# Kernel optimization log

Measured on AMD Instinct MI355X. Metric: run time of the kernel, lower is better.

Reference implementation:

```python
import jax, jax.numpy as jnp
import numpy as np

N = 50000        # nodes
E = 800000       # edges
IN_C = 128       # in_channels
HID = 256        # hidden_channels
HEADS = 4
HD = HID // HEADS
LAYERS = 4
GRAPHS = 64
OUT_C = 32
MAX_POS = 10
EPS = 1e-5


def layer_norm(x, g, b):
    mu = jnp.mean(x, axis=-1, keepdims=True)
    var = jnp.mean((x - mu) ** 2, axis=-1, keepdims=True)
    return (x - mu) / jnp.sqrt(var + EPS) * g + b


def setup_inputs() -> dict:
    key = jax.random.key(0)
    ks = jax.random.split(key, 32)
    s = 0.02
    inp = {
        "x": jax.random.normal(ks[0], (N, IN_C), dtype=jnp.float32),
        "edge_index": jax.random.randint(ks[1], (2, E), 0, N, dtype=jnp.int32),
        "pos_idx": jax.random.randint(ks[2], (N,), 0, MAX_POS, dtype=jnp.int32),
        "batch": jnp.sort(jax.random.randint(ks[3], (N,), 0, GRAPHS, dtype=jnp.int32)),
        # encoder MLP: Linear(IN->HID), ReLU, LN(HID), Linear(HID->HID); weights stored [in,out]
        "enc_w1": jax.random.normal(ks[4], (IN_C, HID)) * s,
        "enc_b1": jnp.zeros((HID,), jnp.float32),
        "enc_g": jnp.ones((HID,), jnp.float32),
        "enc_beta": jnp.zeros((HID,), jnp.float32),
        "enc_w2": jax.random.normal(ks[5], (HID, HID)) * s,
        "enc_b2": jnp.zeros((HID,), jnp.float32),
        "pos_emb": jax.random.normal(ks[6], (MAX_POS, HID)) * s,
        # stacked attention-layer params [LAYERS, ...]
        "Wq": jax.random.normal(ks[7], (LAYERS, HID, HID)) * s,
        "bq": jnp.zeros((LAYERS, HID), jnp.float32),
        "Wk": jax.random.normal(ks[8], (LAYERS, HID, HID)) * s,
        "bk": jnp.zeros((LAYERS, HID), jnp.float32),
        "Wv": jax.random.normal(ks[9], (LAYERS, HID, HID)) * s,
        "bv": jnp.zeros((LAYERS, HID), jnp.float32),
        "mlp_w1": jax.random.normal(ks[10], (LAYERS, 2 * HID, HID)) * s,
        "mlp_b1": jnp.zeros((LAYERS, HID), jnp.float32),
        "mlp_g": jnp.ones((LAYERS, HID), jnp.float32),
        "mlp_beta": jnp.zeros((LAYERS, HID), jnp.float32),
        "mlp_w2": jax.random.normal(ks[11], (LAYERS, HID, HID)) * s,
        "mlp_b2": jnp.zeros((LAYERS, HID), jnp.float32),
        # classifier
        "cls_w1": jax.random.normal(ks[12], (HID, HID)) * s,
        "cls_b1": jnp.zeros((HID,), jnp.float32),
        "cls_g": jnp.ones((HID,), jnp.float32),
        "cls_beta": jnp.zeros((HID,), jnp.float32),
        "cls_w2": jax.random.normal(ks[13], (HID, OUT_C)) * s,
        "cls_b2": jnp.zeros((OUT_C,), jnp.float32),
    }
    return inp


def reference(x, edge_index, pos_idx, batch,
              enc_w1, enc_b1, enc_g, enc_beta, enc_w2, enc_b2, pos_emb,
              Wq, bq, Wk, bk, Wv, bv,
              mlp_w1, mlp_b1, mlp_g, mlp_beta, mlp_w2, mlp_b2,
              cls_w1, cls_b1, cls_g, cls_beta, cls_w2, cls_b2):
    row, col = edge_index[0], edge_index[1]
    n = x.shape[0]
    e = row.shape[0]

    # NodeEncoder
    h = layer_norm(jax.nn.relu(x @ enc_w1 + enc_b1), enc_g, enc_beta) @ enc_w2 + enc_b2
    h = h + pos_emb[pos_idx]

    scale = jnp.asarray(HD, h.dtype) ** 0.5
    for l in range(LAYERS):
        Q = (h @ Wq[l] + bq[l]).reshape(n, HEADS, HD)
        K = (h @ Wk[l] + bk[l]).reshape(n, HEADS, HD)
        V = (h @ Wv[l] + bv[l]).reshape(n, HEADS, HD)
        # per-edge attention scores [E, HEADS]
        scores = jnp.sum(Q[row] * K[col], axis=-1) / scale
        # segment softmax over destination node `row`
        m = jax.ops.segment_max(scores, row, num_segments=n)
        ex = jnp.exp(scores - m[row])
        denom = jax.ops.segment_sum(ex, row, num_segments=n)
        w = ex / denom[row]                         # [E, HEADS]
        msg = (w[..., None] * V[col]).reshape(e, HID)
        agg = jax.ops.segment_sum(msg, row, num_segments=n)  # [N, HID]
        cat = jnp.concatenate([h, agg], axis=-1)
        z = layer_norm(jax.nn.relu(cat @ mlp_w1[l] + mlp_b1[l]), mlp_g[l], mlp_beta[l]) @ mlp_w2[l] + mlp_b2[l]
        h = z + h

    # global mean pool over graphs
    sums = jax.ops.segment_sum(h, batch, num_segments=GRAPHS)
    cnt = jax.ops.segment_sum(jnp.ones((n, 1), h.dtype), batch, num_segments=GRAPHS)
    pooled = sums / jnp.maximum(cnt, 1.0)

    out = layer_norm(jax.nn.relu(pooled @ cls_w1 + cls_b1), cls_g, cls_beta) @ cls_w2 + cls_b2
    return out
```

## Files before the change

### kernel.cpp

```cpp
#include <hip/hip_runtime.h>
#include <cstdint>

#define HID 256
#define HEADS 4
#define GRAPHS 64
#define OUTC 32
#define EPSV 1e-5f
#define PSPLIT 32

typedef __bf16 b16x8 __attribute__((ext_vector_type(8)));
typedef float  f32x4 __attribute__((ext_vector_type(4)));

__device__ __forceinline__ f32x4 mfma16(b16x8 a, b16x8 b, f32x4 c) {
    return __builtin_amdgcn_mfma_f32_16x16x32_bf16(a, b, c, 0, 0, 0);
}

__device__ __forceinline__ unsigned int pack_bf16(float a, float b) {
    unsigned short ua = __builtin_bit_cast(unsigned short, (__bf16)a);
    unsigned short ub = __builtin_bit_cast(unsigned short, (__bf16)b);
    return (unsigned int)ua | ((unsigned int)ub << 16);
}

__device__ __forceinline__ void unpack2(unsigned int u, float& lo, float& hi) {
    lo = __builtin_bit_cast(float, u << 16);
    hi = __builtin_bit_cast(float, u & 0xffff0000u);
}

__global__ __launch_bounds__(256) void wtrans_kernel(const float* __restrict__ W,
    unsigned short* __restrict__ Wt, int K, int C)
{
    __shared__ float tile[32][33];
    const float* Wm = W + (size_t)blockIdx.z * K * C;
    unsigned short* Wtm = Wt + (size_t)blockIdx.z * K * C;
    int k0 = blockIdx.x * 32, c0 = blockIdx.y * 32;
    int tx = threadIdx.x & 31, ty = threadIdx.x >> 5;
#pragma unroll
    for (int i = 0; i < 32; i += 8)
        tile[ty + i][tx] = Wm[(size_t)(k0 + ty + i) * C + c0 + tx];
    __syncthreads();
#pragma unroll
    for (int i = 0; i < 32; i += 8) {
        float v = tile[tx][ty + i];
        Wtm[(size_t)(c0 + ty + i) * K + k0 + tx] =
            __builtin_bit_cast(unsigned short, (__bf16)v);
    }
}

__global__ __launch_bounds__(256) void enc1_mfma(
    const float* __restrict__ in0, const unsigned short* __restrict__ Wt,
    const float* __restrict__ bias, const float* __restrict__ g,
    const float* __restrict__ be, unsigned short* __restrict__ outb, int n)
{
    constexpr int KTILE = 128, ROWB = 256;
    __shared__ __align__(16) char alds[64 * 256];
    __shared__ float red[4][64][2];
    int tid = threadIdx.x, lane = tid & 63, wv = tid >> 6;
    int cg = lane & 15, rg = lane >> 4;
    int base = blockIdx.x * 64;
    int cbase = wv * 64;

    f32x4 acc[4][4];
#pragma unroll
    for (int m = 0; m < 4; m++)
#pragma unroll
        for (int f = 0; f < 4; f++) acc[m][f] = (f32x4){0.f, 0.f, 0.f, 0.f};

#pragma unroll
    for (int i = 0; i < 8; i++) {
        int idx = (i * 256 + tid) * 4;
        int row = idx >> 7, k = idx & 127;
        int node = base + row;
        float4 v = {0.f, 0.f, 0.f, 0.f};
        if (node < n) v = *(const float4*)(in0 + (size_t)node * KTILE + k);
        uint2 pp; pp.x = pack_bf16(v.x, v.y); pp.y = pack_bf16(v.z, v.w);
        int off = row * ROWB + k * 2;
        off ^= (row & 7) << 4;
        *(uint2*)(alds + off) = pp;
    }
    __syncthreads();

#pragma unroll 2
    for (int k0 = 0; k0 < KTILE; k0 += 32) {
        b16x8 a[4], b[4];
#pragma unroll
        for (int m = 0; m < 4; m++) {
            int R = m * 16 + cg;
            int off = R * ROWB + (k0 + rg * 8) * 2;
            off ^= (R & 7) << 4;
            a[m] = __builtin_bit_cast(b16x8, *(const uint4*)(alds + off));
        }
#pragma unroll
        for (int f = 0; f < 4; f++) {
            const unsigned short* p = Wt + (size_t)(cbase + f * 16 + cg) * KTILE + k0 + rg * 8;
            b[f] = __builtin_bit_cast(b16x8, *(const uint4*)p);
        }
#pragma unroll
        for (int m = 0; m < 4; m++)
#pragma unroll
            for (int f = 0; f < 4; f++)
                acc[m][f] = mfma16(a[m], b[f], acc[m][f]);
    }

    float bias_v[4], g_v[4], be_v[4];
#pragma unroll
    for (int f = 0; f < 4; f++) {
        int col = cbase + f * 16 + cg;
        bias_v[f] = bias[col]; g_v[f] = g[col]; be_v[f] = be[col];
    }
#pragma unroll
    for (int m = 0; m < 4; m++)
#pragma unroll
        for (int f = 0; f < 4; f++)
#pragma unroll
            for (int r = 0; r < 4; r++)
                acc[m][f][r] = fmaxf(acc[m][f][r] + bias_v[f], 0.f);
#pragma unroll
    for (int m = 0; m < 4; m++)
#pragma unroll
        for (int r = 0; r < 4; r++) {
            float s = acc[m][0][r] + acc[m][1][r] + acc[m][2][r] + acc[m][3][r];
            float q = acc[m][0][r] * acc[m][0][r] + acc[m][1][r] * acc[m][1][r]
                    + acc[m][2][r] * acc[m][2][r] + acc[m][3][r] * acc[m][3][r];
#pragma unroll
            for (int o = 1; o < 16; o <<= 1) {
                s += __shfl_xor(s, o, 64); q += __shfl_xor(q, o, 64);
            }
            if (cg == 0) { int R = m * 16 + rg * 4 + r; red[wv][R][0] = s; red[wv][R][1] = q; }
        }
    __syncthreads();
#pragma unroll
    for (int m = 0; m < 4; m++)
#pragma unroll
        for (int r = 0; r < 4; r++) {
            int R = m * 16 + rg * 4 + r;
            float S = red[0][R][0] + red[1][R][0] + red[2][R][0] + red[3][R][0];
            float Q = red[0][R][1] + red[1][R][1] + red[2][R][1] + red[3][R][1];
            float mu = S * (1.f / HID);
            float rs = rsqrtf(Q * (1.f / HID) - mu * mu + EPSV);
            int row = base + R;
            if (row >= n) continue;
            size_t ro = (size_t)row * HID;
#pragma unroll
            for (int f = 0; f < 4; f++) {
                float v = (acc[m][f][r] - mu) * rs * g_v[f] + be_v[f];
                outb[ro + cbase + f * 16 + cg] = __builtin_bit_cast(unsigned short, (__bf16)v);
            }
        }
}

template<int KTILE, int NPASS, bool RELU_LN, bool ADD_RES, bool POS, bool OUTF, bool OUTB>
__global__ __launch_bounds__(256) void gemm_bf16(
    const unsigned short* __restrict__ in0, const unsigned short* __restrict__ in1,
    const unsigned short* __restrict__ Wt, const float* __restrict__ bias,
    const float* __restrict__ g, const float* __restrict__ be,
    const float* __restrict__ addsrc, const float* __restrict__ pos_emb,
    const int* __restrict__ pidx, float* __restrict__ outf,
    unsigned short* __restrict__ outb, int n)
{
    constexpr int KS = KTILE * NPASS;
    constexpr int ROWB = KTILE * 2;
    constexpr int UPR = KTILE / 8;
    __shared__ __align__(16) char alds[64 * KTILE * 2];
    __shared__ float red[4][64][2];

    int tid = threadIdx.x, lane = tid & 63, wv = tid >> 6;
    int cg = lane & 15, rg = lane >> 4;
    int base = blockIdx.x * 64;
    int cbase = wv * 64;

    f32x4 acc[4][4];
#pragma unroll
    for (int m = 0; m < 4; m++)
#pragma unroll
        for (int f = 0; f < 4; f++) acc[m][f] = (f32x4){0.f, 0.f, 0.f, 0.f};

    for (int pass = 0; pass < NPASS; pass++) {
        if (pass) __syncthreads();
        const unsigned short* src = pass ? in1 : in0;
        constexpr int ITERS = (64 * UPR) / 256;
#pragma unroll
        for (int i = 0; i < ITERS; i++) {
            int idx = i * 256 + tid;
            int row = idx / UPR, u = idx % UPR;
            int node = base + row;
            uint4 v = {0u, 0u, 0u, 0u};
            if (node < n) v = *(const uint4*)(src + (size_t)node * KTILE + u * 8);
            int off = row * ROWB + u * 16;
            off ^= (row & 7) << 4;
            *(uint4*)(alds + off) = v;
        }
        __syncthreads();

        const unsigned short* Wp = Wt + pass * KTILE;
#pragma unroll 2
        for (int k0 = 0; k0 < KTILE; k0 += 32) {
            b16x8 a[4], b[4];
#pragma unroll
            for (int m = 0; m < 4; m++) {
                int R = m * 16 + cg;
                int off = R * ROWB + (k0 + rg * 8) * 2;
                off ^= (R & 7) << 4;
                a[m] = __builtin_bit_cast(b16x8, *(const uint4*)(alds + off));
            }
#pragma unroll
            for (int f = 0; f < 4; f++) {
                const unsigned short* p = Wp + (size_t)(cbase + f * 16 + cg) * KS + k0 + rg * 8;
                b[f] = __builtin_bit_cast(b16x8, *(const uint4*)p);
            }
#pragma unroll
            for (int m = 0; m < 4; m++)
#pragma unroll
                for (int f = 0; f < 4; f++)
                    acc[m][f] = mfma16(a[m], b[f], acc[m][f]);
        }
    }

    float bias_v[4], g_v[4], be_v[4];
#pragma unroll
    for (int f = 0; f < 4; f++) {
        int col = cbase + f * 16 + cg;
        bias_v[f] = bias[col];
        if (RELU_LN) { g_v[f] = g[col]; be_v[f] = be[col]; }
    }
#pragma unroll
    for (int m = 0; m < 4; m++)
#pragma unroll
        for (int f = 0; f < 4; f++)
#pragma unroll
            for (int r = 0; r < 4; r++) acc[m][f][r] += bias_v[f];

    if (RELU_LN) {
#pragma unroll
        for (int m = 0; m < 4; m++)
#pragma unroll
            for (int f = 0; f < 4; f++)
#pragma unroll
                for (int r = 0; r < 4; r++) acc[m][f][r] = fmaxf(acc[m][f][r], 0.f);
#pragma unroll
        for (int m = 0; m < 4; m++)
#pragma unroll
            for (int r = 0; r < 4; r++) {
                float s = acc[m][0][r] + acc[m][1][r] + acc[m][2][r] + acc[m][3][r];
                float q = acc[m][0][r] * acc[m][0][r] + acc[m][1][r] * acc[m][1][r]
                        + acc[m][2][r] * acc[m][2][r] + acc[m][3][r] * acc[m][3][r];
#pragma unroll
                for (int o = 1; o < 16; o <<= 1) {
                    s += __shfl_xor(s, o, 64); q += __shfl_xor(q, o, 64);
                }
                if (cg == 0) { int R = m * 16 + rg * 4 + r; red[wv][R][0] = s; red[wv][R][1] = q; }
            }
        __syncthreads();
#pragma unroll
        for (int m = 0; m < 4; m++)
#pragma unroll
            for (int r = 0; r < 4; r++) {
                int R = m * 16 + rg * 4 + r;
                float S = red[0][R][0] + red[1][R][0] + red[2][R][0] + red[3][R][0];
                float Q = red[0][R][1] + red[1][R][1] + red[2][R][1] + red[3][R][1];
                float mu = S * (1.f / HID);
                float rs = rsqrtf(Q * (1.f / HID) - mu * mu + EPSV);
#pragma unroll
                for (int f = 0; f < 4; f++)
                    acc[m][f][r] = (acc[m][f][r] - mu) * rs * g_v[f] + be_v[f];
            }
    }

#pragma unroll
    for (int m = 0; m < 4; m++)
#pragma unroll
        for (int r = 0; r < 4; r++) {
            int row = base + m * 16 + rg * 4 + r;
            if (row >= n) continue;
            size_t ro = (size_t)row * HID;
            int pid = 0;
            if (POS) pid = pidx[row];
#pragma unroll
            for (int f = 0; f < 4; f++) {
                int col = cbase + f * 16 + cg;
                float v = acc[m][f][r];
                if (ADD_RES) v += addsrc[ro + col];
                if (POS)     v += pos_emb[(size_t)pid * HID + col];
                if (OUTF)    outf[ro + col] = v;
                if (OUTB)    outb[ro + col] = __builtin_bit_cast(unsigned short, (__bf16)v);
            }
        }
}

__global__ __launch_bounds__(256) void qkv_mfma_kernel(
    const unsigned short* __restrict__ hsrc,
    const unsigned short* __restrict__ Wtq, const unsigned short* __restrict__ Wtk,
    const unsigned short* __restrict__ Wtv,
    const float* __restrict__ bq, const float* __restrict__ bk, const float* __restrict__ bv,
    unsigned short* __restrict__ Qo, unsigned short* __restrict__ Ko,
    unsigned short* __restrict__ Vo, int n)
{
    constexpr int ROWB = 512;
    __shared__ __align__(16) char alds[64 * 512];
    int tid = threadIdx.x, lane = tid & 63, wv = tid >> 6;
    int cg = lane & 15, rg = lane >> 4;
    int base = blockIdx.x * 64;
    int cbase = wv * 64;

#pragma unroll
    for (int i = 0; i < 8; i++) {
        int idx = i * 256 + tid;
        int row = idx >> 5, u = idx & 31;
        int node = base + row;
        uint4 v = {0u, 0u, 0u, 0u};
        if (node < n) v = *(const uint4*)(hsrc + (size_t)node * HID + u * 8);
        int off = row * ROWB + u * 16;
        off ^= (row & 7) << 4;
        *(uint4*)(alds + off) = v;
    }
    __syncthreads();

    for (int mat = 0; mat < 3; mat++) {
        const unsigned short* Wp = (mat == 0) ? Wtq : (mat == 1) ? Wtk : Wtv;
        const float* bp = (mat == 0) ? bq : (mat == 1) ? bk : bv;
        unsigned short* op = (mat == 0) ? Qo : (mat == 1) ? Ko : Vo;

        f32x4 acc[4][4];
#pragma unroll
        for (int m = 0; m < 4; m++)
#pragma unroll
            for (int f = 0; f < 4; f++) acc[m][f] = (f32x4){0.f, 0.f, 0.f, 0.f};

#pragma unroll 2
        for (int k0 = 0; k0 < 256; k0 += 32) {
            b16x8 a[4], b[4];
#pragma unroll
            for (int m = 0; m < 4; m++) {
                int R = m * 16 + cg;
                int off = R * ROWB + (k0 + rg * 8) * 2;
                off ^= (R & 7) << 4;
                a[m] = __builtin_bit_cast(b16x8, *(const uint4*)(alds + off));
            }
#pragma unroll
            for (int f = 0; f < 4; f++) {
                const unsigned short* p = Wp + (size_t)(cbase + f * 16 + cg) * 256 + k0 + rg * 8;
                b[f] = __builtin_bit_cast(b16x8, *(const uint4*)p);
            }
#pragma unroll
            for (int m = 0; m < 4; m++)
#pragma unroll
                for (int f = 0; f < 4; f++)
                    acc[m][f] = mfma16(a[m], b[f], acc[m][f]);
        }

        float bias_v[4];
#pragma unroll
        for (int f = 0; f < 4; f++) bias_v[f] = bp[cbase + f * 16 + cg];
#pragma unroll
        for (int m = 0; m < 4; m++)
#pragma unroll
            for (int r = 0; r < 4; r++) {
                int row = base + m * 16 + rg * 4 + r;
                if (row >= n) continue;
                size_t ro = (size_t)row * HID;
#pragma unroll
                for (int f = 0; f < 4; f++) {
                    float v = acc[m][f][r] + bias_v[f];
                    op[ro + cbase + f * 16 + cg] = __builtin_bit_cast(unsigned short, (__bf16)v);
                }
            }
    }
}

__global__ void count_kernel(const int* __restrict__ row, int* __restrict__ counts, int e)
{
    int i = blockIdx.x * blockDim.x + threadIdx.x;
    if (i < e) atomicAdd(&counts[row[i]], 1);
}

__global__ __launch_bounds__(256) void scan1_kernel(const int* __restrict__ counts,
    int* __restrict__ offs, int* __restrict__ bsum, int n)
{
    __shared__ int wsumS[4];
    int tid = threadIdx.x, b = blockIdx.x;
    int i = b * 256 + tid;
    int v = (i < n) ? counts[i] : 0;
    int lane = tid & 63, wv = tid >> 6;
    int s = v;
#pragma unroll
    for (int o = 1; o < 64; o <<= 1) { int t = __shfl_up(s, o, 64); if (lane >= o) s += t; }
    if (lane == 63) wsumS[wv] = s;
    __syncthreads();
    int add = 0;
    for (int j = 0; j < wv; j++) add += wsumS[j];
    s += add;
    if (i < n) offs[i + 1] = s;
    if (tid == 255) bsum[b] = s;
}

__global__ __launch_bounds__(256) void scan2_kernel(int* __restrict__ bsum, int nb)
{
    __shared__ int wsumS[4];
    int tid = threadIdx.x;
// ... 43 lines not shown
    int hw = (wv << 1) | (lane >> 5);
    int l32 = lane & 31;
    int grp = l32 >> 3;
    int start = offs[node], fin = offs[node + 1];
    if (fin == start) {
        agg[(size_t)node * HID + tid] = 0;
        return;
    }

    uint4 qr = *(const uint4*)(Qm + (size_t)node * HID + l32 * 8);
    float qf[8];
    unpack2(qr.x, qf[0], qf[1]);
    unpack2(qr.y, qf[2], qf[3]);
    unpack2(qr.z, qf[4], qf[5]);
    unpack2(qr.w, qf[6], qf[7]);

    float m = -3.0e38f, d = 0.f;
    float acc[8];
#pragma unroll
    for (int j = 0; j < 8; j++) acc[j] = 0.f;

    for (int i = start + hw; i < fin; i += 8) {
        int c = ccol[i];
        uint4 kr = *(const uint4*)(Km + (size_t)c * HID + l32 * 8);
        float k0, k1, k2, k3, k4, k5, k6, k7;
        unpack2(kr.x, k0, k1); unpack2(kr.y, k2, k3);
        unpack2(kr.z, k4, k5); unpack2(kr.w, k6, k7);
        float p = qf[0] * k0 + qf[1] * k1 + qf[2] * k2 + qf[3] * k3
                + qf[4] * k4 + qf[5] * k5 + qf[6] * k6 + qf[7] * k7;
        p += __shfl_xor(p, 1, 64);
        p += __shfl_xor(p, 2, 64);
        p += __shfl_xor(p, 4, 64);
        float s = p * 0.125f;
        float mn = fmaxf(m, s);
        float sc = __expf(m - mn);
        float w = __expf(s - mn);
        d = d * sc + w;
        uint4 vr = *(const uint4*)(Vm + (size_t)c * HID + l32 * 8);
        float v0, v1, v2, v3, v4, v5, v6, v7;
        unpack2(vr.x, v0, v1); unpack2(vr.y, v2, v3);
        unpack2(vr.z, v4, v5); unpack2(vr.w, v6, v7);
        acc[0] = acc[0] * sc + w * v0;  acc[1] = acc[1] * sc + w * v1;
        acc[2] = acc[2] * sc + w * v2;  acc[3] = acc[3] * sc + w * v3;
        acc[4] = acc[4] * sc + w * v4;  acc[5] = acc[5] * sc + w * v5;
        acc[6] = acc[6] * sc + w * v6;  acc[7] = acc[7] * sc + w * v7;
        m = mn;
    }
    if ((l32 & 7) == 0) { wredM[hw][grp] = m; wredD[hw][grp] = d; }
    __syncthreads();
    float M = wredM[0][grp];
#pragma unroll
    for (int j = 1; j < 8; j++) M = fmaxf(M, wredM[j][grp]);
    float fac = __expf(m - M);
    float4 a0 = {acc[0] * fac, acc[1] * fac, acc[2] * fac, acc[3] * fac};
    float4 a1 = {acc[4] * fac, acc[5] * fac, acc[6] * fac, acc[7] * fac};
    *(float4*)&accT[hw][l32 * 8]     = a0;
    *(float4*)&accT[hw][l32 * 8 + 4] = a1;
    __syncthreads();
    int hh = tid >> 6;
    float M2 = wredM[0][hh];
#pragma unroll
    for (int j = 1; j < 8; j++) M2 = fmaxf(M2, wredM[j][hh]);
    float D = 0.f;
#pragma unroll
    for (int j = 0; j < 8; j++) D += wredD[j][hh] * __expf(wredM[j][hh] - M2);
    float r = 0.f;
#pragma unroll
    for (int j = 0; j < 8; j++) r += accT[j][tid];
    agg[(size_t)node * HID + tid] = __builtin_bit_cast(unsigned short, (__bf16)(r / D));
}

__global__ void bounds_kernel(const int* __restrict__ batch, int* __restrict__ gb, int n)
{
    int g = threadIdx.x;
    if (g > GRAPHS) return;
    int lo = 0, hi = n;
    while (lo < hi) { int mid = (lo + hi) >> 1; if (batch[mid] < g) lo = mid + 1; else hi = mid; }
    gb[g] = lo;
}
// ... 72 lines not shown
    const float* bq       = (const float*)d_in[12];
    const float* Wk       = (const float*)d_in[13];
    const float* bk       = (const float*)d_in[14];
    const float* Wv       = (const float*)d_in[15];
    const float* bv       = (const float*)d_in[16];
    const float* mlp_w1   = (const float*)d_in[17];
    const float* mlp_b1   = (const float*)d_in[18];
    const float* mlp_g    = (const float*)d_in[19];
    const float* mlp_beta = (const float*)d_in[20];
    const float* mlp_w2   = (const float*)d_in[21];
    const float* mlp_b2   = (const float*)d_in[22];
    const float* cls_w1   = (const float*)d_in[23];
    const float* cls_b1   = (const float*)d_in[24];
    const float* cls_g    = (const float*)d_in[25];
    const float* cls_beta = (const float*)d_in[26];
    const float* cls_w2   = (const float*)d_in[27];
    const float* cls_b2   = (const float*)d_in[28];

    int n = in_sizes[2];
    int e = in_sizes[1] / 2;
    const int* row = ei;
    const int* col = ei + e;

    char* p = (char*)d_ws;
    auto alloc = [&](size_t bytes) -> void* {
        void* r = (void*)p;
        p += (bytes + 255) & ~(size_t)255;
        return r;
    };
    size_t NH = (size_t)n * HID;
    float* h             = (float*)alloc(NH * 4);
    unsigned short* h16  = (unsigned short*)alloc(NH * 2);
    unsigned short* a16  = (unsigned short*)alloc(NH * 2);
    unsigned short* m16  = (unsigned short*)alloc(NH * 2);
    unsigned short* Qb   = (unsigned short*)alloc(NH * 2);
    unsigned short* Kb   = (unsigned short*)alloc(NH * 2);
    unsigned short* Vb   = (unsigned short*)alloc(NH * 2);
    float* partial = (float*)alloc((size_t)GRAPHS * PSPLIT * HID * 4);
    float* pooled  = (float*)alloc((size_t)GRAPHS * HID * 4);
    int* counts = (int*)alloc((size_t)n * 4);
    int* offs   = (int*)alloc((size_t)(n + 1) * 4);
    int* cur    = (int*)alloc((size_t)n * 4);
    int* ccol   = (int*)alloc((size_t)e * 4);
    int* bsum   = (int*)alloc(1024);
    int* gb     = (int*)alloc((GRAPHS + 1) * 4);
    unsigned short* wt_e1 = (unsigned short*)alloc((size_t)128 * 256 * 2);
    unsigned short* wt_e2 = (unsigned short*)alloc((size_t)256 * 256 * 2);
    unsigned short* wt_q  = (unsigned short*)alloc((size_t)4 * 256 * 256 * 2);
    unsigned short* wt_k  = (unsigned short*)alloc((size_t)4 * 256 * 256 * 2);
    unsigned short* wt_v  = (unsigned short*)alloc((size_t)4 * 256 * 256 * 2);
    unsigned short* wt_m1 = (unsigned short*)alloc((size_t)4 * 512 * 256 * 2);
    unsigned short* wt_m2 = (unsigned short*)alloc((size_t)4 * 256 * 256 * 2);

    int gblocks = (n + 63) / 64;
    int nb = (n + 255) / 256;

    wtrans_kernel<<<dim3(4, 8, 1),  256, 0, stream>>>(enc_w1, wt_e1, 128, 256);
    wtrans_kernel<<<dim3(8, 8, 1),  256, 0, stream>>>(enc_w2, wt_e2, 256, 256);
    wtrans_kernel<<<dim3(8, 8, 4),  256, 0, stream>>>(Wq,     wt_q,  256, 256);
    wtrans_kernel<<<dim3(8, 8, 4),  256, 0, stream>>>(Wk,     wt_k,  256, 256);
    wtrans_kernel<<<dim3(8, 8, 4),  256, 0, stream>>>(Wv,     wt_v,  256, 256);
    wtrans_kernel<<<dim3(16, 8, 4), 256, 0, stream>>>(mlp_w1, wt_m1, 512, 256);
    wtrans_kernel<<<dim3(8, 8, 4),  256, 0, stream>>>(mlp_w2, wt_m2, 256, 256);

    hipMemsetAsync(counts, 0, (size_t)n * 4, stream);
    hipMemsetAsync(cur, 0, (size_t)n * 4, stream);
    count_kernel<<<(e + 255) / 256, 256, 0, stream>>>(row, counts, e);
    scan1_kernel<<<nb, 256, 0, stream>>>(counts, offs, bsum, n);
    scan2_kernel<<<1, 256, 0, stream>>>(bsum, nb);
    scan3_kernel<<<nb, 256, 0, stream>>>(offs, bsum, n);
    scatter_kernel<<<(e + 255) / 256, 256, 0, stream>>>(row, col, offs, cur, ccol, e);
    bounds_kernel<<<1, 128, 0, stream>>>(batch, gb, n);

    enc1_mfma<<<gblocks, 256, 0, stream>>>(x, wt_e1, enc_b1, enc_g, enc_beta, m16, n);
    gemm_bf16<256, 1, false, false, true, true, true><<<gblocks, 256, 0, stream>>>(
        m16, nullptr, wt_e2, enc_b2, nullptr, nullptr, nullptr, pos_emb, pidx, h, h16, n);

    for (int l = 0; l < 4; l++) {
        size_t wo = (size_t)l * 256 * 256;
        size_t bo = (size_t)l * HID;
        qkv_mfma_kernel<<<gblocks, 256, 0, stream>>>(
            h16, wt_q + wo, wt_k + wo, wt_v + wo, bq + bo, bk + bo, bv + bo,
            Qb, Kb, Vb, n);
        attn_bf16_kernel<<<n, 256, 0, stream>>>(Qb, Kb, Vb, offs, ccol, a16, n);
        gemm_bf16<256, 2, true, false, false, false, true><<<gblocks, 256, 0, stream>>>(
            h16, a16, wt_m1 + (size_t)l * 512 * 256, mlp_b1 + bo,
            mlp_g + bo, mlp_beta + bo, nullptr, nullptr, nullptr, nullptr, m16, n);
        gemm_bf16<256, 1, false, true, false, true, true><<<gblocks, 256, 0, stream>>>(
            m16, nullptr, wt_m2 + wo, mlp_b2 + bo, nullptr, nullptr, h, nullptr, nullptr,
            h, h16, n);
    }

    pool_partial_kernel<<<dim3(PSPLIT, GRAPHS), 256, 0, stream>>>(h, gb, partial);
    pool_reduce_kernel<<<GRAPHS, 256, 0, stream>>>(partial, gb, pooled);
    cls_kernel<<<GRAPHS, 256, 0, stream>>>(pooled, cls_w1, cls_b1, cls_g, cls_beta,
                                           cls_w2, cls_b2, (float*)d_out);
}
```

Baseline: 1.419 ms.

## Fuse encoder, per-layer MLP and next-layer QKV GEMMs into single kernels

The two encoder GEMMs and the first QKV projection become one kernel, and each layer's two MLP GEMMs plus the next layer's QKV projection become another. Intermediate tiles stay in LDS instead of being written to and re-read from global memory, and several launches per layer are dropped. Separately, the online softmax in the attention kernel now rescales its accumulators only when the running max rises by more than 8, which skips most rescale multiplies. The cost is a longer serial kernel per block with larger LDS use, and the lazy rescale lets the exp weights grow up to e^8 before renormalising.

Result: slower. 1.495 ms (+5.3%).

```diff
diff --git a/kernel.cpp b/kernel.cpp
--- a/kernel.cpp
+++ b/kernel.cpp
@@ -26,72 +26,38 @@
     hi = __builtin_bit_cast(float, u & 0xffff0000u);
 }
 
-__global__ __launch_bounds__(256) void wtrans_kernel(const float* __restrict__ W,
-    unsigned short* __restrict__ Wt, int K, int C)
-{
-    __shared__ float tile[32][33];
-    const float* Wm = W + (size_t)blockIdx.z * K * C;
-    unsigned short* Wtm = Wt + (size_t)blockIdx.z * K * C;
-    int k0 = blockIdx.x * 32, c0 = blockIdx.y * 32;
-    int tx = threadIdx.x & 31, ty = threadIdx.x >> 5;
-#pragma unroll
-    for (int i = 0; i < 32; i += 8)
-        tile[ty + i][tx] = Wm[(size_t)(k0 + ty + i) * C + c0 + tx];
-    __syncthreads();
-#pragma unroll
-    for (int i = 0; i < 32; i += 8) {
-        float v = tile[tx][ty + i];
-        Wtm[(size_t)(c0 + ty + i) * K + k0 + tx] =
-            __builtin_bit_cast(unsigned short, (__bf16)v);
-    }
-}
-
-__global__ __launch_bounds__(256) void enc1_mfma(
-    const float* __restrict__ in0, const unsigned short* __restrict__ Wt,
-    const float* __restrict__ bias, const float* __restrict__ g,
-    const float* __restrict__ be, unsigned short* __restrict__ outb, int n)
-{
-    constexpr int KTILE = 128, ROWB = 256;
-    __shared__ __align__(16) char alds[64 * 256];
-    __shared__ float red[4][64][2];
-    int tid = threadIdx.x, lane = tid & 63, wv = tid >> 6;
-    int cg = lane & 15, rg = lane >> 4;
-    int base = blockIdx.x * 64;
-    int cbase = wv * 64;
-
-    f32x4 acc[4][4];
-#pragma unroll
-    for (int m = 0; m < 4; m++)
-#pragma unroll
-        for (int f = 0; f < 4; f++) acc[m][f] = (f32x4){0.f, 0.f, 0.f, 0.f};
-
+__device__ __forceinline__ void stage_b16(char* buf, const unsigned short* src,
+                                          int base, int n, int tid)
+{
 #pragma unroll
     for (int i = 0; i < 8; i++) {
-        int idx = (i * 256 + tid) * 4;
-        int row = idx >> 7, k = idx & 127;
+        int idx = i * 256 + tid;
+        int row = idx >> 5, u = idx & 31;
         int node = base + row;
-        float4 v = {0.f, 0.f, 0.f, 0.f};
-        if (node < n) v = *(const float4*)(in0 + (size_t)node * KTILE + k);
-        uint2 pp; pp.x = pack_bf16(v.x, v.y); pp.y = pack_bf16(v.z, v.w);
-        int off = row * ROWB + k * 2;
+        uint4 v = {0u, 0u, 0u, 0u};
+        if (node < n) v = *(const uint4*)(src + (size_t)node * HID + u * 8);
+        int off = row * 512 + u * 16;
         off ^= (row & 7) << 4;
-        *(uint2*)(alds + off) = pp;
-    }
-    __syncthreads();
-
+        *(uint4*)(buf + off) = v;
+    }
+}
+
+__device__ __forceinline__ void pass256(const char* buf, const unsigned short* Wt,
+    int KS, int cbase, int cg, int rg, f32x4 (&acc)[4][4])
+{
 #pragma unroll 2
-    for (int k0 = 0; k0 < KTILE; k0 += 32) {
+    for (int k0 = 0; k0 < 256; k0 += 32) {
         b16x8 a[4], b[4];
 #pragma unroll
         for (int m = 0; m < 4; m++) {
             int R = m * 16 + cg;
-            int off = R * ROWB + (k0 + rg * 8) * 2;
+            int off = R * 512 + (k0 + rg * 8) * 2;
             off ^= (R & 7) << 4;
-            a[m] = __builtin_bit_cast(b16x8, *(const uint4*)(alds + off));
+            a[m] = __builtin_bit_cast(b16x8, *(const uint4*)(buf + off));
         }
 #pragma unroll
         for (int f = 0; f < 4; f++) {
-            const unsigned short* p = Wt + (size_t)(cbase + f * 16 + cg) * KTILE + k0 + rg * 8;
+            const unsigned short* p = Wt + (size_t)(cbase + f * 16 + cg) * KS + k0 + rg * 8;
             b[f] = __builtin_bit_cast(b16x8, *(const uint4*)p);
         }
 #pragma unroll
@@ -100,12 +66,16 @@
             for (int f = 0; f < 4; f++)
                 acc[m][f] = mfma16(a[m], b[f], acc[m][f]);
     }
-
-    float bias_v[4], g_v[4], be_v[4];
+}
+
+__device__ __forceinline__ void tile_bias_relu_ln(f32x4 (&acc)[4][4], float (*red)[64][2],
+    const float* bias, const float* g, const float* be, int cbase, int cg, int rg, int wv)
+{
+    float b_v[4], g_v[4], be_v[4];
 #pragma unroll
     for (int f = 0; f < 4; f++) {
         int col = cbase + f * 16 + cg;
-        bias_v[f] = bias[col]; g_v[f] = g[col]; be_v[f] = be[col];
+        b_v[f] = bias[col]; g_v[f] = g[col]; be_v[f] = be[col];
     }
 #pragma unroll
     for (int m = 0; m < 4; m++)
@@ -113,7 +83,7 @@
         for (int f = 0; f < 4; f++)
 #pragma unroll
             for (int r = 0; r < 4; r++)
-                acc[m][f][r] = fmaxf(acc[m][f][r] + bias_v[f], 0.f);
+                acc[m][f][r] = fmaxf(acc[m][f][r] + b_v[f], 0.f);
 #pragma unroll
     for (int m = 0; m < 4; m++)
 #pragma unroll
@@ -137,216 +107,154 @@
             float Q = red[0][R][1] + red[1][R][1] + red[2][R][1] + red[3][R][1];
             float mu = S * (1.f / HID);
             float rs = rsqrtf(Q * (1.f / HID) - mu * mu + EPSV);
-            int row = base + R;
-            if (row >= n) continue;
-            size_t ro = (size_t)row * HID;
+#pragma unroll
+            for (int f = 0; f < 4; f++)
+                acc[m][f][r] = (acc[m][f][r] - mu) * rs * g_v[f] + be_v[f];
+        }
+}
+
+__device__ __forceinline__ void put_tile(char* buf, const f32x4 (&acc)[4][4],
+    int cbase, int cg, int rg)
+{
+#pragma unroll
+    for (int m = 0; m < 4; m++)
+#pragma unroll
+        for (int r = 0; r < 4; r++) {
+            int R = m * 16 + rg * 4 + r;
 #pragma unroll
             for (int f = 0; f < 4; f++) {
-                float v = (acc[m][f][r] - mu) * rs * g_v[f] + be_v[f];
-                outb[ro + cbase + f * 16 + cg] = __builtin_bit_cast(unsigned short, (__bf16)v);
+                int col = cbase + f * 16 + cg;
+                int off = R * 512 + col * 2;
+                off ^= (R & 7) << 4;
+                *(unsigned short*)(buf + off) =
+                    __builtin_bit_cast(unsigned short, (__bf16)acc[m][f][r]);
             }
         }
 }
 
-template<int KTILE, int NPASS, bool RELU_LN, bool ADD_RES, bool POS, bool OUTF, bool OUTB>
-__global__ __launch_bounds__(256) void gemm_bf16(
-    const unsigned short* __restrict__ in0, const unsigned short* __restrict__ in1,
-    const unsigned short* __restrict__ Wt, const float* __restrict__ bias,
-    const float* __restrict__ g, const float* __restrict__ be,
-    const float* __restrict__ addsrc, const float* __restrict__ pos_emb,
-    const int* __restrict__ pidx, float* __restrict__ outf,
-    unsigned short* __restrict__ outb, int n)
-{
-    constexpr int KS = KTILE * NPASS;
-    constexpr int ROWB = KTILE * 2;
-    constexpr int UPR = KTILE / 8;
-    __shared__ __align__(16) char alds[64 * KTILE * 2];
+__device__ __forceinline__ void zero_acc(f32x4 (&acc)[4][4])
+{
+#pragma unroll
+    for (int m = 0; m < 4; m++)
+#pragma unroll
+        for (int f = 0; f < 4; f++) acc[m][f] = (f32x4){0.f, 0.f, 0.f, 0.f};
+}
+
+__global__ __launch_bounds__(256) void wtrans_kernel(const float* __restrict__ W,
+    unsigned short* __restrict__ Wt, int K, int C)
+{
+    __shared__ float tile[32][33];
+    const float* Wm = W + (size_t)blockIdx.z * K * C;
+    unsigned short* Wtm = Wt + (size_t)blockIdx.z * K * C;
+    int k0 = blockIdx.x * 32, c0 = blockIdx.y * 32;
+    int tx = threadIdx.x & 31, ty = threadIdx.x >> 5;
+#pragma unroll
+    for (int i = 0; i < 32; i += 8)
+        tile[ty + i][tx] = Wm[(size_t)(k0 + ty + i) * C + c0 + tx];
+    __syncthreads();
+#pragma unroll
+    for (int i = 0; i < 32; i += 8) {
+        float v = tile[tx][ty + i];
+        Wtm[(size_t)(c0 + ty + i) * K + k0 + tx] =
+            __builtin_bit_cast(unsigned short, (__bf16)v);
+    }
+}
+
+__global__ __launch_bounds__(256) void enc_fused(
+    const float* __restrict__ x,
+    const unsigned short* __restrict__ wt_e1, const float* __restrict__ eb1,
+    const float* __restrict__ eg, const float* __restrict__ ebe,
+    const unsigned short* __restrict__ wt_e2, const float* __restrict__ eb2,
+    const float* __restrict__ pos_emb, const int* __restrict__ pidx,
+    const unsigned short* __restrict__ wtq, const unsigned short* __restrict__ wtk,
+    const unsigned short* __restrict__ wtv,
+    const float* __restrict__ bqv, const float* __restrict__ bkv, const float* __restrict__ bvv,
+    float* __restrict__ h, unsigned short* __restrict__ h16,
+    unsigned short* __restrict__ Qo, unsigned short* __restrict__ Ko,
+    unsigned short* __restrict__ Vo, int n)
+{
+    __shared__ __align__(16) char buf[64 * 512];
     __shared__ float red[4][64][2];
-
     int tid = threadIdx.x, lane = tid & 63, wv = tid >> 6;
     int cg = lane & 15, rg = lane >> 4;
     int base = blockIdx.x * 64;
     int cbase = wv * 64;
 
+#pragma unroll
+    for (int i = 0; i < 8; i++) {
+        int idx = (i * 256 + tid) * 4;
+        int row = idx >> 7, k = idx & 127;
+        int node = base + row;
+        float4 v = {0.f, 0.f, 0.f, 0.f};
+        if (node < n) v = *(const float4*)(x + (size_t)node * 128 + k);
+        uint2 pp; pp.x = pack_bf16(v.x, v.y); pp.y = pack_bf16(v.z, v.w);
+        int off = row * 256 + k * 2;
+        off ^= (row & 7) << 4;
+        *(uint2*)(buf + off) = pp;
+    }
+    __syncthreads();
+
     f32x4 acc[4][4];
-#pragma unroll
-    for (int m = 0; m < 4; m++)
-#pragma unroll
-        for (int f = 0; f < 4; f++) acc[m][f] = (f32x4){0.f, 0.f, 0.f, 0.f};
-
-    for (int pass = 0; pass < NPASS; pass++) {
-        if (pass) __syncthreads();
-        const unsigned short* src = pass ? in1 : in0;
-        constexpr int ITERS = (64 * UPR) / 256;
-#pragma unroll
-        for (int i = 0; i < ITERS; i++) {
-            int idx = i * 256 + tid;
-            int row = idx / UPR, u = idx % UPR;
-            int node = base + row;
-            uint4 v = {0u, 0u, 0u, 0u};
-            if (node < n) v = *(const uint4*)(src + (size_t)node * KTILE + u * 8);
-            int off = row * ROWB + u * 16;
-            off ^= (row & 7) << 4;
-            *(uint4*)(alds + off) = v;
-        }
-        __syncthreads();
-
-        const unsigned short* Wp = Wt + pass * KTILE;
+    zero_acc(acc);
 #pragma unroll 2
-        for (int k0 = 0; k0 < KTILE; k0 += 32) {
-            b16x8 a[4], b[4];
-#pragma unroll
-            for (int m = 0; m < 4; m++) {
-                int R = m * 16 + cg;
-                int off = R * ROWB + (k0 + rg * 8) * 2;
-                off ^= (R & 7) << 4;
-                a[m] = __builtin_bit_cast(b16x8, *(const uint4*)(alds + off));
-            }
-#pragma unroll
-            for (int f = 0; f < 4; f++) {
-                const unsigned short* p = Wp + (size_t)(cbase + f * 16 + cg) * KS + k0 + rg * 8;
-                b[f] = __builtin_bit_cast(b16x8, *(const uint4*)p);
-            }
-#pragma unroll
-            for (int m = 0; m < 4; m++)
-#pragma unroll
-                for (int f = 0; f < 4; f++)
-                    acc[m][f] = mfma16(a[m], b[f], acc[m][f]);
-        }
-    }
-
-    float bias_v[4], g_v[4], be_v[4];
-#pragma unroll
-    for (int f = 0; f < 4; f++) {
-        int col = cbase + f * 16 + cg;
-        bias_v[f] = bias[col];
-        if (RELU_LN) { g_v[f] = g[col]; be_v[f] = be[col]; }
-    }
-#pragma unroll
-    for (int m = 0; m < 4; m++)
-#pragma unroll
-        for (int f = 0; f < 4; f++)
-#pragma unroll
-            for (int r = 0; r < 4; r++) acc[m][f][r] += bias_v[f];
-
-    if (RELU_LN) {
+    for (int k0 = 0; k0 < 128; k0 += 32) {
+        b16x8 a[4], b[4];
+#pragma unroll
+        for (int m = 0; m < 4; m++) {
+            int R = m * 16 + cg;
+            int off = R * 256 + (k0 + rg * 8) * 2;
+            off ^= (R & 7) << 4;
+            a[m] = __builtin_bit_cast(b16x8, *(const uint4*)(buf + off));
+        }
+#pragma unroll
+        for (int f = 0; f < 4; f++) {
+            const unsigned short* p = wt_e1 + (size_t)(cbase + f * 16 + cg) * 128 + k0 + rg * 8;
+            b[f] = __builtin_bit_cast(b16x8, *(const uint4*)p);
+        }
 #pragma unroll
         for (int m = 0; m < 4; m++)
 #pragma unroll
             for (int f = 0; f < 4; f++)
-#pragma unroll
-                for (int r = 0; r < 4; r++) acc[m][f][r] = fmaxf(acc[m][f][r], 0.f);
-#pragma unroll
-        for (int m = 0; m < 4; m++)
-#pragma unroll
-            for (int r = 0; r < 4; r++) {
-                float s = acc[m][0][r] + acc[m][1][r] + acc[m][2][r] + acc[m][3][r];
-                float q = acc[m][0][r] * acc[m][0][r] + acc[m][1][r] * acc[m][1][r]
-                        + acc[m][2][r] * acc[m][2][r] + acc[m][3][r] * acc[m][3][r];
-#pragma unroll
-                for (int o = 1; o < 16; o <<= 1) {
-                    s += __shfl_xor(s, o, 64); q += __shfl_xor(q, o, 64);
-                }
-                if (cg == 0) { int R = m * 16 + rg * 4 + r; red[wv][R][0] = s; red[wv][R][1] = q; }
-            }
-        __syncthreads();
-#pragma unroll
-        for (int m = 0; m < 4; m++)
-#pragma unroll
-            for (int r = 0; r < 4; r++) {
-                int R = m * 16 + rg * 4 + r;
-                float S = red[0][R][0] + red[1][R][0] + red[2][R][0] + red[3][R][0];
-                float Q = red[0][R][1] + red[1][R][1] + red[2][R][1] + red[3][R][1];
-                float mu = S * (1.f / HID);
-                float rs = rsqrtf(Q * (1.f / HID) - mu * mu + EPSV);
-#pragma unroll
-                for (int f = 0; f < 4; f++)
-                    acc[m][f][r] = (acc[m][f][r] - mu) * rs * g_v[f] + be_v[f];
-            }
-    }
-
+                acc[m][f] = mfma16(a[m], b[f], acc[m][f]);
+    }
+    tile_bias_relu_ln(acc, red, eb1, eg, ebe, cbase, cg, rg, wv);
+    put_tile(buf, acc, cbase, cg, rg);
+    __syncthreads();
+
+    zero_acc(acc);
+    pass256(buf, wt_e2, 256, cbase, cg, rg, acc);
+    float b2_v[4];
+#pragma unroll
+    for (int f = 0; f < 4; f++) b2_v[f] = eb2[cbase + f * 16 + cg];
 #pragma unroll
     for (int m = 0; m < 4; m++)
 #pragma unroll
         for (int r = 0; r < 4; r++) {
             int row = base + m * 16 + rg * 4 + r;
-            if (row >= n) continue;
+            bool ok = row < n;
+            int pid = ok ? pidx[row] : 0;
             size_t ro = (size_t)row * HID;
-            int pid = 0;
-            if (POS) pid = pidx[row];
 #pragma unroll
             for (int f = 0; f < 4; f++) {
                 int col = cbase + f * 16 + cg;
-                float v = acc[m][f][r];
-                if (ADD_RES) v += addsrc[ro + col];
-                if (POS)     v += pos_emb[(size_t)pid * HID + col];
-                if (OUTF)    outf[ro + col] = v;
-                if (OUTB)    outb[ro + col] = __builtin_bit_cast(unsigned short, (__bf16)v);
+                float v = acc[m][f][r] + b2_v[f] + pos_emb[(size_t)pid * HID + col];
+                acc[m][f][r] = v;
+                if (ok) {
+                    h[ro + col] = v;
+                    h16[ro + col] = __builtin_bit_cast(unsigned short, (__bf16)v);
+                }
             }
         }
-}
-
-__global__ __launch_bounds__(256) void qkv_mfma_kernel(
-    const unsigned short* __restrict__ hsrc,
-    const unsigned short* __restrict__ Wtq, const unsigned short* __restrict__ Wtk,
-    const unsigned short* __restrict__ Wtv,
-    const float* __restrict__ bq, const float* __restrict__ bk, const float* __restrict__ bv,
-    unsigned short* __restrict__ Qo, unsigned short* __restrict__ Ko,
-    unsigned short* __restrict__ Vo, int n)
-{
-    constexpr int ROWB = 512;
-    __shared__ __align__(16) char alds[64 * 512];
-    int tid = threadIdx.x, lane = tid & 63, wv = tid >> 6;
-    int cg = lane & 15, rg = lane >> 4;
-    int base = blockIdx.x * 64;
-    int cbase = wv * 64;
-
-#pragma unroll
-    for (int i = 0; i < 8; i++) {
-        int idx = i * 256 + tid;
-        int row = idx >> 5, u = idx & 31;
-        int node = base + row;
-        uint4 v = {0u, 0u, 0u, 0u};
-        if (node < n) v = *(const uint4*)(hsrc + (size_t)node * HID + u * 8);
-        int off = row * ROWB + u * 16;
-        off ^= (row & 7) << 4;
-        *(uint4*)(alds + off) = v;
-    }
+    __syncthreads();
+    put_tile(buf, acc, cbase, cg, rg);
     __syncthreads();
 
     for (int mat = 0; mat < 3; mat++) {
-        const unsigned short* Wp = (mat == 0) ? Wtq : (mat == 1) ? Wtk : Wtv;
-        const float* bp = (mat == 0) ? bq : (mat == 1) ? bk : bv;
+        const unsigned short* Wp = (mat == 0) ? wtq : (mat == 1) ? wtk : wtv;
+        const float* bp = (mat == 0) ? bqv : (mat == 1) ? bkv : bvv;
         unsigned short* op = (mat == 0) ? Qo : (mat == 1) ? Ko : Vo;
-
-        f32x4 acc[4][4];
-#pragma unroll
-        for (int m = 0; m < 4; m++)
-#pragma unroll
-            for (int f = 0; f < 4; f++) acc[m][f] = (f32x4){0.f, 0.f, 0.f, 0.f};
-
-#pragma unroll 2
-        for (int k0 = 0; k0 < 256; k0 += 32) {
-            b16x8 a[4], b[4];
-#pragma unroll
-            for (int m = 0; m < 4; m++) {
-                int R = m * 16 + cg;
-                int off = R * ROWB + (k0 + rg * 8) * 2;
-                off ^= (R & 7) << 4;
-                a[m] = __builtin_bit_cast(b16x8, *(const uint4*)(alds + off));
-            }
-#pragma unroll
-            for (int f = 0; f < 4; f++) {
-                const unsigned short* p = Wp + (size_t)(cbase + f * 16 + cg) * 256 + k0 + rg * 8;
-                b[f] = __builtin_bit_cast(b16x8, *(const uint4*)p);
-            }
-#pragma unroll
-            for (int m = 0; m < 4; m++)
-#pragma unroll
-                for (int f = 0; f < 4; f++)
-                    acc[m][f] = mfma16(a[m], b[f], acc[m][f]);
-        }
-
+        zero_acc(acc);
+        pass256(buf, Wp, 256, cbase, cg, rg, acc);
         float bias_v[4];
 #pragma unroll
         for (int f = 0; f < 4; f++) bias_v[f] = bp[cbase + f * 16 + cg];
@@ -363,6 +271,94 @@
                     op[ro + cbase + f * 16 + cg] = __builtin_bit_cast(unsigned short, (__bf16)v);
                 }
             }
+    }
+}
+
+template<bool HAS_QKV>
+__global__ __launch_bounds__(256) void layer_fused(
+    unsigned short* __restrict__ h16, const unsigned short* __restrict__ a16,
+    const unsigned short* __restrict__ wt_m1, const float* __restrict__ b1,
+    const float* __restrict__ g, const float* __restrict__ be,
+    const unsigned short* __restrict__ wt_m2, const float* __restrict__ b2,
+    float* __restrict__ h,
+    const unsigned short* __restrict__ wtq, const unsigned short* __restrict__ wtk,
+    const unsigned short* __restrict__ wtv,
+    const float* __restrict__ bqv, const float* __restrict__ bkv, const float* __restrict__ bvv,
+    unsigned short* __restrict__ Qo, unsigned short* __restrict__ Ko,
+    unsigned short* __restrict__ Vo, int n)
+{
+    __shared__ __align__(16) char buf[64 * 512];
+    __shared__ float red[4][64][2];
+    int tid = threadIdx.x, lane = tid & 63, wv = tid >> 6;
+    int cg = lane & 15, rg = lane >> 4;
+    int base = blockIdx.x * 64;
+    int cbase = wv * 64;
+
+    f32x4 acc[4][4];
+    zero_acc(acc);
+
+    stage_b16(buf, h16, base, n, tid);
+    __syncthreads();
+    pass256(buf, wt_m1, 512, cbase, cg, rg, acc);
+    __syncthreads();
+    stage_b16(buf, a16, base, n, tid);
+    __syncthreads();
+    pass256(buf, wt_m1 + 256, 512, cbase, cg, rg, acc);
+
+    tile_bias_relu_ln(acc, red, b1, g, be, cbase, cg, rg, wv);
+    put_tile(buf, acc, cbase, cg, rg);
+    __syncthreads();
+
+    zero_acc(acc);
+    pass256(buf, wt_m2, 256, cbase, cg, rg, acc);
+    float b2_v[4];
+#pragma unroll
+    for (int f = 0; f < 4; f++) b2_v[f] = b2[cbase + f * 16 + cg];
+#pragma unroll
+    for (int m = 0; m < 4; m++)
+#pragma unroll
+        for (int r = 0; r < 4; r++) {
+            int row = base + m * 16 + rg * 4 + r;
+            if (row >= n) continue;
+            size_t ro = (size_t)row * HID;
+#pragma unroll
+            for (int f = 0; f < 4; f++) {
+                int col = cbase + f * 16 + cg;
+                float v = acc[m][f][r] + b2_v[f] + h[ro + col];
+                acc[m][f][r] = v;
+                h[ro + col] = v;
+                h16[ro + col] = __builtin_bit_cast(unsigned short, (__bf16)v);
+            }
+        }
+
+    if constexpr (HAS_QKV) {
+        __syncthreads();
+        put_tile(buf, acc, cbase, cg, rg);
+        __syncthreads();
+        for (int mat = 0; mat < 3; mat++) {
+            const unsigned short* Wp = (mat == 0) ? wtq : (mat == 1) ? wtk : wtv;
+            const float* bp = (mat == 0) ? bqv : (mat == 1) ? bkv : bvv;
+            unsigned short* op = (mat == 0) ? Qo : (mat == 1) ? Ko : Vo;
+            zero_acc(acc);
+            pass256(buf, Wp, 256, cbase, cg, rg, acc);
+            float bias_v[4];
+#pragma unroll
+            for (int f = 0; f < 4; f++) bias_v[f] = bp[cbase + f * 16 + cg];
+#pragma unroll
+            for (int m = 0; m < 4; m++)
+#pragma unroll
+                for (int r = 0; r < 4; r++) {
+                    int row = base + m * 16 + rg * 4 + r;
+                    if (row >= n) continue;
+                    size_t ro = (size_t)row * HID;
+#pragma unroll
+                    for (int f = 0; f < 4; f++) {
+                        float v = acc[m][f][r] + bias_v[f];
+                        op[ro + cbase + f * 16 + cg] =
+                            __builtin_bit_cast(unsigned short, (__bf16)v);
+                    }
+                }
+        }
     }
 }
 
@@ -472,19 +468,23 @@
         p += __shfl_xor(p, 2, 64);
         p += __shfl_xor(p, 4, 64);
         float s = p * 0.125f;
-        float mn = fmaxf(m, s);
-        float sc = __expf(m - mn);
-        float w = __expf(s - mn);
-        d = d * sc + w;
+        if (s > m + 8.f) {
+            float sc = __expf(m - s);
+            d *= sc;
+#pragma unroll
+            for (int j = 0; j < 8; j++) acc[j] *= sc;
+            m = s;
+        }
+        float w = __expf(s - m);
+        d += w;
         uint4 vr = *(const uint4*)(Vm + (size_t)c * HID + l32 * 8);
         float v0, v1, v2, v3, v4, v5, v6, v7;
         unpack2(vr.x, v0, v1); unpack2(vr.y, v2, v3);
         unpack2(vr.z, v4, v5); unpack2(vr.w, v6, v7);
-        acc[0] = acc[0] * sc + w * v0;  acc[1] = acc[1] * sc + w * v1;
-        acc[2] = acc[2] * sc + w * v2;  acc[3] = acc[3] * sc + w * v3;
-        acc[4] = acc[4] * sc + w * v4;  acc[5] = acc[5] * sc + w * v5;
-        acc[6] = acc[6] * sc + w * v6;  acc[7] = acc[7] * sc + w * v7;
-        m = mn;
+        acc[0] += w * v0;  acc[1] += w * v1;
+        acc[2] += w * v2;  acc[3] += w * v3;
+        acc[4] += w * v4;  acc[5] += w * v5;
+        acc[6] += w * v6;  acc[7] += w * v7;
     }
     if ((l32 & 7) == 0) { wredM[hw][grp] = m; wredD[hw][grp] = d; }
     __syncthreads();
@@ -623,7 +623,6 @@
     float* h             = (float*)alloc(NH * 4);
     unsigned short* h16  = (unsigned short*)alloc(NH * 2);
     unsigned short* a16  = (unsigned short*)alloc(NH * 2);
-    unsigned short* m16  = (unsigned short*)alloc(NH * 2);
     unsigned short* Qb   = (unsigned short*)alloc(NH * 2);
     unsigned short* Kb   = (unsigned short*)alloc(NH * 2);
     unsigned short* Vb   = (unsigned short*)alloc(NH * 2);
@@ -663,23 +662,31 @@
     scatter_kernel<<<(e + 255) / 256, 256, 0, stream>>>(row, col, offs, cur, ccol, e);
     bounds_kernel<<<1, 128, 0, stream>>>(batch, gb, n);
 
-    enc1_mfma<<<gblocks, 256, 0, stream>>>(x, wt_e1, enc_b1, enc_g, enc_beta, m16, n);
-    gemm_bf16<256, 1, false, false, true, true, true><<<gblocks, 256, 0, stream>>>(
-        m16, nullptr, wt_e2, enc_b2, nullptr, nullptr, nullptr, pos_emb, pidx, h, h16, n);
+    enc_fused<<<gblocks, 256, 0, stream>>>(
+        x, wt_e1, enc_b1, enc_g, enc_beta, wt_e2, enc_b2, pos_emb, pidx,
+        wt_q, wt_k, wt_v, bq, bk, bv,
+        h, h16, Qb, Kb, Vb, n);
 
     for (int l = 0; l < 4; l++) {
-        size_t wo = (size_t)l * 256 * 256;
-        size_t bo = (size_t)l * HID;
-        qkv_mfma_kernel<<<gblocks, 256, 0, stream>>>(
-            h16, wt_q + wo, wt_k + wo, wt_v + wo, bq + bo, bk + bo, bv + bo,
-            Qb, Kb, Vb, n);
+        size_t wo1 = (size_t)l * 512 * 256;
+        size_t wo  = (size_t)l * 256 * 256;
+        size_t bo  = (size_t)l * HID;
         attn_bf16_kernel<<<n, 256, 0, stream>>>(Qb, Kb, Vb, offs, ccol, a16, n);
-        gemm_bf16<256, 2, true, false, false, false, true><<<gblocks, 256, 0, stream>>>(
-            h16, a16, wt_m1 + (size_t)l * 512 * 256, mlp_b1 + bo,
-            mlp_g + bo, mlp_beta + bo, nullptr, nullptr, nullptr, nullptr, m16, n);
-        gemm_bf16<256, 1, false, true, false, true, true><<<gblocks, 256, 0, stream>>>(
-            m16, nullptr, wt_m2 + wo, mlp_b2 + bo, nullptr, nullptr, h, nullptr, nullptr,
-            h, h16, n);
+        if (l < 3) {
+            size_t wn = (size_t)(l + 1) * 256 * 256;
+            size_t bn = (size_t)(l + 1) * HID;
+            layer_fused<true><<<gblocks, 256, 0, stream>>>(
+                h16, a16, wt_m1 + wo1, mlp_b1 + bo, mlp_g + bo, mlp_beta + bo,
+                wt_m2 + wo, mlp_b2 + bo, h,
+                wt_q + wn, wt_k + wn, wt_v + wn, bq + bn, bk + bn, bv + bn,
+                Qb, Kb, Vb, n);
+        } else {
+            layer_fused<false><<<gblocks, 256, 0, stream>>>(
+                h16, a16, wt_m1 + wo1, mlp_b1 + bo, mlp_g + bo, mlp_beta + bo,
+                wt_m2 + wo, mlp_b2 + bo, h,
+                nullptr, nullptr, nullptr, nullptr, nullptr, nullptr,
+                nullptr, nullptr, nullptr, n);
+        }
     }
 
     pool_partial_kernel<<<dim3(PSPLIT, GRAPHS), 256, 0, stream>>>(h, gb, partial);
```

## Preload weight fragments into registers and use lazy rescaling in online softmax

Applied to the files above, without the earlier changes.

The GEMM kernels (encoder, generic bf16 GEMM, QKV) now load every weight B-fragment for the whole K range into registers before the MFMA loop. The loop is fully unrolled, so these global loads are issued early and overlap with the LDS staging of activations. Launch bounds are raised to a minimum of 2 blocks per SM to constrain register use. The edge-attention online softmax only rescales the running max and accumulators when a new score exceeds the current max by more than 8, which removes two exps and a multiply per element on most edges. The cost is much higher VGPR pressure (up to 128 extra registers in QKV, with possible spills under the 2-block bound) and a divergent branch in the softmax.

New measurement: 1.498 ms. +5.6%, slower.

```diff
diff --git a/kernel.cpp b/kernel.cpp
--- a/kernel.cpp
+++ b/kernel.cpp
@@ -46,7 +46,7 @@
     }
 }
 
-__global__ __launch_bounds__(256) void enc1_mfma(
+__global__ __launch_bounds__(256, 2) void enc1_mfma(
     const float* __restrict__ in0, const unsigned short* __restrict__ Wt,
     const float* __restrict__ bias, const float* __restrict__ g,
     const float* __restrict__ be, unsigned short* __restrict__ outb, int n)
@@ -59,11 +59,13 @@
     int base = blockIdx.x * 64;
     int cbase = wv * 64;
 
-    f32x4 acc[4][4];
-#pragma unroll
-    for (int m = 0; m < 4; m++)
-#pragma unroll
-        for (int f = 0; f < 4; f++) acc[m][f] = (f32x4){0.f, 0.f, 0.f, 0.f};
+    b16x8 w[4][4];
+#pragma unroll
+    for (int kk = 0; kk < 4; kk++)
+#pragma unroll
+        for (int f = 0; f < 4; f++)
+            w[kk][f] = __builtin_bit_cast(b16x8, *(const uint4*)(
+                Wt + (size_t)(cbase + f * 16 + cg) * KTILE + kk * 32 + rg * 8));
 
 #pragma unroll
     for (int i = 0; i < 8; i++) {
@@ -79,26 +81,27 @@
     }
     __syncthreads();
 
-#pragma unroll 2
-    for (int k0 = 0; k0 < KTILE; k0 += 32) {
-        b16x8 a[4], b[4];
+    f32x4 acc[4][4];
+#pragma unroll
+    for (int m = 0; m < 4; m++)
+#pragma unroll
+        for (int f = 0; f < 4; f++) acc[m][f] = (f32x4){0.f, 0.f, 0.f, 0.f};
+
+#pragma unroll
+    for (int kk = 0; kk < 4; kk++) {
+        b16x8 a[4];
 #pragma unroll
         for (int m = 0; m < 4; m++) {
             int R = m * 16 + cg;
-            int off = R * ROWB + (k0 + rg * 8) * 2;
+            int off = R * ROWB + (kk * 32 + rg * 8) * 2;
             off ^= (R & 7) << 4;
             a[m] = __builtin_bit_cast(b16x8, *(const uint4*)(alds + off));
         }
 #pragma unroll
-        for (int f = 0; f < 4; f++) {
-            const unsigned short* p = Wt + (size_t)(cbase + f * 16 + cg) * KTILE + k0 + rg * 8;
-            b[f] = __builtin_bit_cast(b16x8, *(const uint4*)p);
-        }
-#pragma unroll
         for (int m = 0; m < 4; m++)
 #pragma unroll
             for (int f = 0; f < 4; f++)
-                acc[m][f] = mfma16(a[m], b[f], acc[m][f]);
+                acc[m][f] = mfma16(a[m], w[kk][f], acc[m][f]);
     }
 
     float bias_v[4], g_v[4], be_v[4];
@@ -149,7 +152,7 @@
 }
 
 template<int KTILE, int NPASS, bool RELU_LN, bool ADD_RES, bool POS, bool OUTF, bool OUTB>
-__global__ __launch_bounds__(256) void gemm_bf16(
+__global__ __launch_bounds__(256, 2) void gemm_bf16(
     const unsigned short* __restrict__ in0, const unsigned short* __restrict__ in1,
     const unsigned short* __restrict__ Wt, const float* __restrict__ bias,
     const float* __restrict__ g, const float* __restrict__ be,
@@ -160,6 +163,7 @@
     constexpr int KS = KTILE * NPASS;
     constexpr int ROWB = KTILE * 2;
     constexpr int UPR = KTILE / 8;
+    constexpr int NKK = KTILE / 32;
     __shared__ __align__(16) char alds[64 * KTILE * 2];
     __shared__ float red[4][64][2];
 
@@ -177,6 +181,16 @@
     for (int pass = 0; pass < NPASS; pass++) {
         if (pass) __syncthreads();
         const unsigned short* src = pass ? in1 : in0;
+        const unsigned short* Wp = Wt + pass * KTILE;
+
+        b16x8 w[NKK][4];
+#pragma unroll
+        for (int kk = 0; kk < NKK; kk++)
+#pragma unroll
+            for (int f = 0; f < 4; f++)
+                w[kk][f] = __builtin_bit_cast(b16x8, *(const uint4*)(
+                    Wp + (size_t)(cbase + f * 16 + cg) * KS + kk * 32 + rg * 8));
+
         constexpr int ITERS = (64 * UPR) / 256;
 #pragma unroll
         for (int i = 0; i < ITERS; i++) {
@@ -191,27 +205,21 @@
         }
         __syncthreads();
 
-        const unsigned short* Wp = Wt + pass * KTILE;
-#pragma unroll 2
-        for (int k0 = 0; k0 < KTILE; k0 += 32) {
-            b16x8 a[4], b[4];
+#pragma unroll
+        for (int kk = 0; kk < NKK; kk++) {
+            b16x8 a[4];
 #pragma unroll
             for (int m = 0; m < 4; m++) {
                 int R = m * 16 + cg;
-                int off = R * ROWB + (k0 + rg * 8) * 2;
+                int off = R * ROWB + (kk * 32 + rg * 8) * 2;
                 off ^= (R & 7) << 4;
                 a[m] = __builtin_bit_cast(b16x8, *(const uint4*)(alds + off));
             }
 #pragma unroll
-            for (int f = 0; f < 4; f++) {
-                const unsigned short* p = Wp + (size_t)(cbase + f * 16 + cg) * KS + k0 + rg * 8;
-                b[f] = __builtin_bit_cast(b16x8, *(const uint4*)p);
-            }
-#pragma unroll
             for (int m = 0; m < 4; m++)
 #pragma unroll
                 for (int f = 0; f < 4; f++)
-                    acc[m][f] = mfma16(a[m], b[f], acc[m][f]);
+                    acc[m][f] = mfma16(a[m], w[kk][f], acc[m][f]);
         }
     }
 
@@ -286,7 +294,7 @@
         }
 }
 
-__global__ __launch_bounds__(256) void qkv_mfma_kernel(
+__global__ __launch_bounds__(256, 2) void qkv_mfma_kernel(
     const unsigned short* __restrict__ hsrc,
     const unsigned short* __restrict__ Wtq, const unsigned short* __restrict__ Wtk,
     const unsigned short* __restrict__ Wtv,
@@ -319,32 +327,35 @@
         const float* bp = (mat == 0) ? bq : (mat == 1) ? bk : bv;
         unsigned short* op = (mat == 0) ? Qo : (mat == 1) ? Ko : Vo;
 
+        b16x8 w[8][4];
+#pragma unroll
+        for (int kk = 0; kk < 8; kk++)
+#pragma unroll
+            for (int f = 0; f < 4; f++)
+                w[kk][f] = __builtin_bit_cast(b16x8, *(const uint4*)(
+                    Wp + (size_t)(cbase + f * 16 + cg) * 256 + kk * 32 + rg * 8));
+
         f32x4 acc[4][4];
 #pragma unroll
         for (int m = 0; m < 4; m++)
 #pragma unroll
             for (int f = 0; f < 4; f++) acc[m][f] = (f32x4){0.f, 0.f, 0.f, 0.f};
 
-#pragma unroll 2
-        for (int k0 = 0; k0 < 256; k0 += 32) {
-            b16x8 a[4], b[4];
+#pragma unroll
+        for (int kk = 0; kk < 8; kk++) {
+            b16x8 a[4];
 #pragma unroll
             for (int m = 0; m < 4; m++) {
                 int R = m * 16 + cg;
-                int off = R * ROWB + (k0 + rg * 8) * 2;
+                int off = R * ROWB + (kk * 32 + rg * 8) * 2;
                 off ^= (R & 7) << 4;
                 a[m] = __builtin_bit_cast(b16x8, *(const uint4*)(alds + off));
             }
 #pragma unroll
-            for (int f = 0; f < 4; f++) {
-                const unsigned short* p = Wp + (size_t)(cbase + f * 16 + cg) * 256 + k0 + rg * 8;
-                b[f] = __builtin_bit_cast(b16x8, *(const uint4*)p);
-            }
-#pragma unroll
             for (int m = 0; m < 4; m++)
 #pragma unroll
                 for (int f = 0; f < 4; f++)
-                    acc[m][f] = mfma16(a[m], b[f], acc[m][f]);
+                    acc[m][f] = mfma16(a[m], w[kk][f], acc[m][f]);
         }
 
         float bias_v[4];
@@ -472,19 +483,23 @@
         p += __shfl_xor(p, 2, 64);
         p += __shfl_xor(p, 4, 64);
         float s = p * 0.125f;
-        float mn = fmaxf(m, s);
-        float sc = __expf(m - mn);
-        float w = __expf(s - mn);
-        d = d * sc + w;
+        if (s > m + 8.f) {
+            float sc = __expf(m - s);
+            d *= sc;
+#pragma unroll
+            for (int j = 0; j < 8; j++) acc[j] *= sc;
+            m = s;
+        }
+        float w = __expf(s - m);
+        d += w;
         uint4 vr = *(const uint4*)(Vm + (size_t)c * HID + l32 * 8);
         float v0, v1, v2, v3, v4, v5, v6, v7;
         unpack2(vr.x, v0, v1); unpack2(vr.y, v2, v3);
         unpack2(vr.z, v4, v5); unpack2(vr.w, v6, v7);
-        acc[0] = acc[0] * sc + w * v0;  acc[1] = acc[1] * sc + w * v1;
-        acc[2] = acc[2] * sc + w * v2;  acc[3] = acc[3] * sc + w * v3;
-        acc[4] = acc[4] * sc + w * v4;  acc[5] = acc[5] * sc + w * v5;
-        acc[6] = acc[6] * sc + w * v6;  acc[7] = acc[7] * sc + w * v7;
-        m = mn;
+        acc[0] += w * v0;  acc[1] += w * v1;
+        acc[2] += w * v2;  acc[3] += w * v3;
+        acc[4] += w * v4;  acc[5] += w * v5;
+        acc[6] += w * v6;  acc[7] += w * v7;
     }
     if ((l32 & 7) == 0) { wredM[hw][grp] = m; wredD[hw][grp] = d; }
     __syncthreads();
```
